# Optimization experiments

Hardware: AMD Instinct MI355X
Metric: run time of the kernel (lower is better)

Reference implementation:

```python
import jax, jax.numpy as jnp
import numpy as np
import math

B, S, D = 16, 2048, 64


def setup_inputs() -> dict:
    key = jax.random.key(0)
    k1, k2, k3 = jax.random.split(key, 3)
    Q = jax.random.normal(k1, (B, S, D), dtype=jnp.float32)
    K = jax.random.normal(k2, (B, S, D), dtype=jnp.float32)
    V = jax.random.normal(k3, (B, S, D), dtype=jnp.float32)
    # causal mask: True where attention is disallowed (strict upper triangle)
    mask = jnp.triu(jnp.ones((S, S), dtype=bool), k=1)
    mask = jnp.broadcast_to(mask, (B, S, S))
    return {"Q": Q, "K": K, "V": V, "mask": mask, "dk": 64}


def reference(Q, K, V, mask, dk):
    # w = Q K^T / sqrt(dk), masked fill with -1e8
    w = jnp.einsum("bqd,bkd->bqk", Q, K) / math.sqrt(dk)
    w = jnp.where(mask, jnp.float32(-1.0e8), w)
    # distance_func in the original returns 0 (constant, under no_grad),
    # so exp(-1e8 * 0) * w == w; output is softmax of masked scaled scores.
    distance_score = jnp.float32(0.0)
    s = jnp.exp(jnp.float32(-1.0e8) * distance_score) * w
    a = jax.nn.softmax(s, axis=-1)
    return a
```

## Files before the change

### kernel.cpp

```cpp
#include <hip/hip_runtime.h>

using bf16x8 = __attribute__((ext_vector_type(8))) short;
using u16x8  = __attribute__((ext_vector_type(8))) unsigned short;
using f32x4  = __attribute__((ext_vector_type(4))) float;

static constexpr int S  = 2048;
static constexpr int D  = 64;
static constexpr int TQ = 64;
static constexpr float QSCALE = 0.18033688f;

__device__ __forceinline__ unsigned short bf16_rne(float x) {
    unsigned u = __builtin_bit_cast(unsigned, x);
    u += 0x7FFFu + ((u >> 16) & 1u);
    return (unsigned short)(u >> 16);
}
__device__ __forceinline__ float bf16_f32(unsigned short h) {
    unsigned u = ((unsigned)h) << 16;
    return __builtin_bit_cast(float, u);
}
__device__ __forceinline__ f32x4 mfma16(bf16x8 a, bf16x8 b, f32x4 c) {
    return __builtin_amdgcn_mfma_f32_16x16x32_bf16(a, b, c, 0, 0, 0);
}
__device__ __forceinline__ void lbar() {
    asm volatile("s_waitcnt lgkmcnt(0)" ::: "memory");
    __builtin_amdgcn_s_barrier();
    asm volatile("" ::: "memory");
}

__global__ __launch_bounds__(512, 1)
void monotonic_attn(const float* __restrict__ Qg, const float* __restrict__ Kg,
                    float* __restrict__ out)
{
    __shared__ unsigned short qlds[8192];
    __shared__ unsigned short kls[8][2][1024];
    __shared__ float red[8][64];

    const int bid  = blockIdx.x;
    const int wid  = (bid & 7) * ((int)gridDim.x >> 3) + (bid >> 3);
    const int b    = wid >> 4;
    const int pair = wid & 15;

    const int tid = threadIdx.x, lane = tid & 63, wv = tid >> 6;
    const int l15 = lane & 15, g = lane >> 4;

    const float* __restrict__ Qb = Qg + (size_t)b * S * D;
    const float* __restrict__ Kb = Kg + (size_t)b * S * D;
    float* __restrict__ outb = out + (size_t)b * (size_t)S * S;

    const int srow  = lane >> 2;
    const int scp   = lane & 3;
    const int woff0 = srow * 64 + (((scp << 1)    ) ^ (srow & 7)) * 8;
    const int woff1 = srow * 64 + (((scp << 1) | 1) ^ (srow & 7)) * 8;
    const int roff0 = l15 * 64 + ((g    ) ^ (l15 & 7)) * 8;
    const int roff1 = l15 * 64 + ((4 | g) ^ (l15 & 7)) * 8;

    for (int half = 0; half < 2; ++half) {
        const int qt   = half ? pair : 31 - pair;
        const int q0   = qt * TQ;
        const int kend = q0 + TQ;
        const int nC   = kend >> 4;
        const int ni   = (nC - wv + 7) >> 3;

        lbar();
        {
            const int qrow = tid >> 3, qcp = tid & 7;
            const float4* src = reinterpret_cast<const float4*>(Qb + (size_t)(q0 + qrow) * D + qcp * 8);
            const float4 f0 = src[0], f1 = src[1];
            float v[8];
            *reinterpret_cast<float4*>(&v[0]) = f0;
            *reinterpret_cast<float4*>(&v[4]) = f1;
            u16x8 hv, lv;
            #pragma unroll
            for (int i = 0; i < 8; ++i) {
                const float s = v[i] * QSCALE;
                const unsigned short hb = bf16_rne(s);
                hv[i] = hb;
                lv[i] = bf16_rne(s - bf16_f32(hb));
            }
            const int off = qrow * 64 + (qcp ^ (qrow & 7)) * 8;
            *reinterpret_cast<u16x8*>(&qlds[off])        = hv;
            *reinterpret_cast<u16x8*>(&qlds[4096 + off]) = lv;
        }
        lbar();

        bf16x8 qhi[4][2], qlo[4][2];
        #pragma unroll
        for (int qs = 0; qs < 4; ++qs) {
            const int row = qs * 16 + l15;
            #pragma unroll
            for (int c = 0; c < 2; ++c) {
                const int off = row * 64 + ((((c << 2) | g)) ^ (row & 7)) * 8;
                qhi[qs][c] = *reinterpret_cast<const bf16x8*>(&qlds[off]);
                qlo[qs][c] = *reinterpret_cast<const bf16x8*>(&qlds[4096 + off]);
            }
        }

        float inv4[4];
        for (int pass = 0; pass < 2; ++pass) {
            float rsum[4] = {0.f, 0.f, 0.f, 0.f};

            float4 ra0, ra1, ra2, ra3, rb0, rb1, rb2, rb3;
            auto issueA = [&](int i) {
                const int c = wv + (i << 3);
                const float4* p4 = reinterpret_cast<const float4*>(Kb) + (c << 8) + (lane << 2);
                ra0 = p4[0]; ra1 = p4[1]; ra2 = p4[2]; ra3 = p4[3];
            };
            auto issueB = [&](int i) {
                const int c = wv + (i << 3);
                const float4* p4 = reinterpret_cast<const float4*>(Kb) + (c << 8) + (lane << 2);
                rb0 = p4[0]; rb1 = p4[1]; rb2 = p4[2]; rb3 = p4[3];
            };
            auto stage = [&](int i, const float4& x0, const float4& x1,
                             const float4& x2, const float4& x3) {
                float v[16];
                *reinterpret_cast<float4*>(&v[0])  = x0;
                *reinterpret_cast<float4*>(&v[4])  = x1;
                *reinterpret_cast<float4*>(&v[8])  = x2;
                *reinterpret_cast<float4*>(&v[12]) = x3;
                u16x8 h0, h1;
                #pragma unroll
                for (int j = 0; j < 8; ++j) {
                    h0[j] = bf16_rne(v[j]);
                    h1[j] = bf16_rne(v[8 + j]);
                }
                unsigned short* bp = &kls[wv][i & 1][0];
                *reinterpret_cast<u16x8*>(&bp[woff0]) = h0;
                *reinterpret_cast<u16x8*>(&bp[woff1]) = h1;
            };
            auto comp = [&](int i) {
                const unsigned short* bp = &kls[wv][i & 1][0];
                const bf16x8 kf0 = *reinterpret_cast<const bf16x8*>(&bp[roff0]);
                const bf16x8 kf1 = *reinterpret_cast<const bf16x8*>(&bp[roff1]);
                const int klo = (wv + (i << 3)) << 4;
                const int kb  = klo + g * 4;
                #pragma unroll
                for (int qs = 0; qs < 4; ++qs) {
                    const int qmin = q0 + qs * 16, qg = qmin + l15;
                    if (pass == 0) {
                        if (klo > qmin + 15) continue;
                        f32x4 acc = {0.f, 0.f, 0.f, 0.f};
                        acc = mfma16(kf0, qhi[qs][0], acc);
                        acc = mfma16(kf1, qhi[qs][1], acc);
                        acc = mfma16(kf0, qlo[qs][0], acc);
                        acc = mfma16(kf1, qlo[qs][1], acc);
                        if (klo + 15 <= qmin) {
                            rsum[qs] += exp2f(acc[0]) + exp2f(acc[1]) + exp2f(acc[2]) + exp2f(acc[3]);
                        } else {
                            #pragma unroll
                            for (int r = 0; r < 4; ++r)
                                rsum[qs] += (kb + r <= qg) ? exp2f(acc[r]) : 0.f;
                        }
                    } else {
                        f32x4 ov = {0.f, 0.f, 0.f, 0.f};
                        if (klo <= qmin + 15) {
                            f32x4 acc = {0.f, 0.f, 0.f, 0.f};
                            acc = mfma16(kf0, qhi[qs][0], acc);
                            acc = mfma16(kf1, qhi[qs][1], acc);
                            acc = mfma16(kf0, qlo[qs][0], acc);
                            acc = mfma16(kf1, qlo[qs][1], acc);
                            if (klo + 15 <= qmin) {
                                ov[0] = exp2f(acc[0]) * inv4[qs];
                                ov[1] = exp2f(acc[1]) * inv4[qs];
                                ov[2] = exp2f(acc[2]) * inv4[qs];
                                ov[3] = exp2f(acc[3]) * inv4[qs];
                            } else {
                                ov[0] = (kb + 0 <= qg) ? exp2f(acc[0]) * inv4[qs] : 0.f;
                                ov[1] = (kb + 1 <= qg) ? exp2f(acc[1]) * inv4[qs] : 0.f;
                                ov[2] = (kb + 2 <= qg) ? exp2f(acc[2]) * inv4[qs] : 0.f;
                                ov[3] = (kb + 3 <= qg) ? exp2f(acc[3]) * inv4[qs] : 0.f;
                            }
                        }
                        *reinterpret_cast<f32x4*>(outb + (size_t)qg * S + kb) = ov;
                    }
                }
            };

            if (ni > 0) issueA(0);
            if (ni > 1) issueB(1);
            int i = 0;
            for (; i + 2 <= ni; i += 2) {
                stage(i, ra0, ra1, ra2, ra3);
                if (i + 2 < ni) issueA(i + 2);
                comp(i);
                stage(i + 1, rb0, rb1, rb2, rb3);
                if (i + 3 < ni) issueB(i + 3);
                comp(i + 1);
            }
            if (i < ni) { stage(i, ra0, ra1, ra2, ra3); comp(i); }

            if (pass == 0) {
                #pragma unroll
                for (int qs = 0; qs < 4; ++qs) {
                    float v = rsum[qs];
                    v += __shfl_xor(v, 16);
                    v += __shfl_xor(v, 32);
                    if (g == 0) red[wv][qs * 16 + l15] = v;
                }
                lbar();
                #pragma unroll
                for (int qs = 0; qs < 4; ++qs) {
                    const int qi = qs * 16 + l15;
                    inv4[qs] = 1.f / (red[0][qi] + red[1][qi] + red[2][qi] + red[3][qi]
                                    + red[4][qi] + red[5][qi] + red[6][qi] + red[7][qi]);
                }
            }
        }

        {
            f32x4 z = {0.f, 0.f, 0.f, 0.f};
            const size_t rb = (size_t)(q0 + (tid >> 3)) * S;
            for (int cc = kend + (tid & 7) * 4; cc < S; cc += 32)
                *reinterpret_cast<f32x4*>(&outb[rb + cc]) = z;
        }
    }
}

extern "C" void kernel_launch(void* const* d_in, const int* in_sizes, int n_in,
                              void* d_out, int out_size, void* d_ws, size_t ws_size,
                              hipStream_t stream)
{
    const float* Q = (const float*)d_in[0];
    const float* K = (const float*)d_in[1];
    float* out     = (float*)d_out;
    const int nb   = in_sizes[0] / (S * D);

    monotonic_attn<<<dim3(nb * 16), dim3(512), 0, stream>>>(Q, K, out);
}
```

Baseline: 67.43 us.

## Process 32-key chunks per wave iteration and use nontemporal output stores

Each wave now stages and computes two 16-key subtiles (32 keys) per iteration instead of one. This doubles the K loads in flight and halves the loop and barrier overhead per key. The output stores, including the zero fill of the masked region, become nontemporal so the large streaming output does not pollute the caches. The cost is higher register and LDS use, plus coarser causal-boundary granularity that adds some wasted work on diagonal chunks.

```diff
diff --git a/kernel.cpp b/kernel.cpp
--- a/kernel.cpp
+++ b/kernel.cpp
@@ -32,7 +32,7 @@
                     float* __restrict__ out)
 {
     __shared__ unsigned short qlds[8192];
-    __shared__ unsigned short kls[8][2][1024];
+    __shared__ unsigned short kls[8][2][2048];
     __shared__ float red[8][64];
 
     const int bid  = blockIdx.x;
@@ -51,14 +51,20 @@
     const int scp   = lane & 3;
     const int woff0 = srow * 64 + (((scp << 1)    ) ^ (srow & 7)) * 8;
     const int woff1 = srow * 64 + (((scp << 1) | 1) ^ (srow & 7)) * 8;
-    const int roff0 = l15 * 64 + ((g    ) ^ (l15 & 7)) * 8;
-    const int roff1 = l15 * 64 + ((4 | g) ^ (l15 & 7)) * 8;
+    int koff[2][2];
+    #pragma unroll
+    for (int s2 = 0; s2 < 2; ++s2) {
+        const int row = s2 * 16 + l15;
+        koff[s2][0] = row * 64 + ((g    ) ^ (row & 7)) * 8;
+        koff[s2][1] = row * 64 + ((4 | g) ^ (row & 7)) * 8;
+    }
 
     for (int half = 0; half < 2; ++half) {
         const int qt   = half ? pair : 31 - pair;
         const int q0   = qt * TQ;
+        const int qmax = q0 + 63;
         const int kend = q0 + TQ;
-        const int nC   = kend >> 4;
+        const int nC   = kend >> 5;
         const int ni   = (nC - wv + 7) >> 3;
 
         lbar();
@@ -99,78 +105,118 @@
         for (int pass = 0; pass < 2; ++pass) {
             float rsum[4] = {0.f, 0.f, 0.f, 0.f};
 
-            float4 ra0, ra1, ra2, ra3, rb0, rb1, rb2, rb3;
+            float4 ra0, ra1, ra2, ra3, ra4, ra5, ra6, ra7;
+            float4 rb0, rb1, rb2, rb3, rb4, rb5, rb6, rb7;
             auto issueA = [&](int i) {
                 const int c = wv + (i << 3);
-                const float4* p4 = reinterpret_cast<const float4*>(Kb) + (c << 8) + (lane << 2);
-                ra0 = p4[0]; ra1 = p4[1]; ra2 = p4[2]; ra3 = p4[3];
+                const float4* p = reinterpret_cast<const float4*>(Kb) + ((size_t)c << 9) + (lane << 2);
+                ra0 = p[0]; ra1 = p[1]; ra2 = p[2]; ra3 = p[3];
+                ra4 = p[256]; ra5 = p[257]; ra6 = p[258]; ra7 = p[259];
             };
             auto issueB = [&](int i) {
                 const int c = wv + (i << 3);
-                const float4* p4 = reinterpret_cast<const float4*>(Kb) + (c << 8) + (lane << 2);
-                rb0 = p4[0]; rb1 = p4[1]; rb2 = p4[2]; rb3 = p4[3];
+                const float4* p = reinterpret_cast<const float4*>(Kb) + ((size_t)c << 9) + (lane << 2);
+                rb0 = p[0]; rb1 = p[1]; rb2 = p[2]; rb3 = p[3];
+                rb4 = p[256]; rb5 = p[257]; rb6 = p[258]; rb7 = p[259];
             };
             auto stage = [&](int i, const float4& x0, const float4& x1,
-                             const float4& x2, const float4& x3) {
+                             const float4& x2, const float4& x3,
+                             const float4& x4, const float4& x5,
+                             const float4& x6, const float4& x7) {
+                unsigned short* bp = &kls[wv][i & 1][0];
                 float v[16];
+                u16x8 h0, h1;
                 *reinterpret_cast<float4*>(&v[0])  = x0;
                 *reinterpret_cast<float4*>(&v[4])  = x1;
                 *reinterpret_cast<float4*>(&v[8])  = x2;
                 *reinterpret_cast<float4*>(&v[12]) = x3;
-                u16x8 h0, h1;
-                #pragma unroll
-                for (int j = 0; j < 8; ++j) {
-                    h0[j] = bf16_rne(v[j]);
-                    h1[j] = bf16_rne(v[8 + j]);
-                }
-                unsigned short* bp = &kls[wv][i & 1][0];
+                #pragma unroll
+                for (int j = 0; j < 8; ++j) { h0[j] = bf16_rne(v[j]); h1[j] = bf16_rne(v[8 + j]); }
                 *reinterpret_cast<u16x8*>(&bp[woff0]) = h0;
                 *reinterpret_cast<u16x8*>(&bp[woff1]) = h1;
+                *reinterpret_cast<float4*>(&v[0])  = x4;
+                *reinterpret_cast<float4*>(&v[4])  = x5;
+                *reinterpret_cast<float4*>(&v[8])  = x6;
+                *reinterpret_cast<float4*>(&v[12]) = x7;
+                #pragma unroll
+                for (int j = 0; j < 8; ++j) { h0[j] = bf16_rne(v[j]); h1[j] = bf16_rne(v[8 + j]); }
+                *reinterpret_cast<u16x8*>(&bp[woff0 + 1024]) = h0;
+                *reinterpret_cast<u16x8*>(&bp[woff1 + 1024]) = h1;
             };
             auto comp = [&](int i) {
                 const unsigned short* bp = &kls[wv][i & 1][0];
-                const bf16x8 kf0 = *reinterpret_cast<const bf16x8*>(&bp[roff0]);
-                const bf16x8 kf1 = *reinterpret_cast<const bf16x8*>(&bp[roff1]);
-                const int klo = (wv + (i << 3)) << 4;
-                const int kb  = klo + g * 4;
+                const bf16x8 k00 = *reinterpret_cast<const bf16x8*>(&bp[koff[0][0]]);
+                const bf16x8 k01 = *reinterpret_cast<const bf16x8*>(&bp[koff[0][1]]);
+                const bf16x8 k10 = *reinterpret_cast<const bf16x8*>(&bp[koff[1][0]]);
+                const bf16x8 k11 = *reinterpret_cast<const bf16x8*>(&bp[koff[1][1]]);
+                const int kbase = (wv + (i << 3)) << 5;
                 #pragma unroll
                 for (int qs = 0; qs < 4; ++qs) {
                     const int qmin = q0 + qs * 16, qg = qmin + l15;
                     if (pass == 0) {
-                        if (klo > qmin + 15) continue;
-                        f32x4 acc = {0.f, 0.f, 0.f, 0.f};
-                        acc = mfma16(kf0, qhi[qs][0], acc);
-                        acc = mfma16(kf1, qhi[qs][1], acc);
-                        acc = mfma16(kf0, qlo[qs][0], acc);
-                        acc = mfma16(kf1, qlo[qs][1], acc);
-                        if (klo + 15 <= qmin) {
-                            rsum[qs] += exp2f(acc[0]) + exp2f(acc[1]) + exp2f(acc[2]) + exp2f(acc[3]);
-                        } else {
-                            #pragma unroll
-                            for (int r = 0; r < 4; ++r)
-                                rsum[qs] += (kb + r <= qg) ? exp2f(acc[r]) : 0.f;
-                        }
-                    } else {
-                        f32x4 ov = {0.f, 0.f, 0.f, 0.f};
-                        if (klo <= qmin + 15) {
+                        #pragma unroll
+                        for (int s2 = 0; s2 < 2; ++s2) {
+                            const int klo = kbase + s2 * 16;
+                            if (klo > qmin + 15) continue;
+                            const bf16x8 kf0 = s2 ? k10 : k00;
+                            const bf16x8 kf1 = s2 ? k11 : k01;
                             f32x4 acc = {0.f, 0.f, 0.f, 0.f};
                             acc = mfma16(kf0, qhi[qs][0], acc);
                             acc = mfma16(kf1, qhi[qs][1], acc);
                             acc = mfma16(kf0, qlo[qs][0], acc);
                             acc = mfma16(kf1, qlo[qs][1], acc);
                             if (klo + 15 <= qmin) {
-                                ov[0] = exp2f(acc[0]) * inv4[qs];
-                                ov[1] = exp2f(acc[1]) * inv4[qs];
-                                ov[2] = exp2f(acc[2]) * inv4[qs];
-                                ov[3] = exp2f(acc[3]) * inv4[qs];
+                                rsum[qs] += exp2f(acc[0]) + exp2f(acc[1]) + exp2f(acc[2]) + exp2f(acc[3]);
                             } else {
-                                ov[0] = (kb + 0 <= qg) ? exp2f(acc[0]) * inv4[qs] : 0.f;
-                                ov[1] = (kb + 1 <= qg) ? exp2f(acc[1]) * inv4[qs] : 0.f;
-                                ov[2] = (kb + 2 <= qg) ? exp2f(acc[2]) * inv4[qs] : 0.f;
-                                ov[3] = (kb + 3 <= qg) ? exp2f(acc[3]) * inv4[qs] : 0.f;
+                                const int kb = klo + g * 4;
+                                #pragma unroll
+                                for (int r = 0; r < 4; ++r)
+                                    rsum[qs] += (kb + r <= qg) ? exp2f(acc[r]) : 0.f;
                             }
                         }
-                        *reinterpret_cast<f32x4*>(outb + (size_t)qg * S + kb) = ov;
+                    } else {
+                        f32x4 ov0 = {0.f, 0.f, 0.f, 0.f}, ov1 = {0.f, 0.f, 0.f, 0.f};
+                        if (kbase <= qmin + 15) {
+                            f32x4 acc = {0.f, 0.f, 0.f, 0.f};
+                            acc = mfma16(k00, qhi[qs][0], acc);
+                            acc = mfma16(k01, qhi[qs][1], acc);
+                            acc = mfma16(k00, qlo[qs][0], acc);
+                            acc = mfma16(k01, qlo[qs][1], acc);
+                            if (kbase + 15 <= qmin) {
+                                ov0[0] = exp2f(acc[0]) * inv4[qs];
+                                ov0[1] = exp2f(acc[1]) * inv4[qs];
+                                ov0[2] = exp2f(acc[2]) * inv4[qs];
+                                ov0[3] = exp2f(acc[3]) * inv4[qs];
+                            } else {
+                                const int kb = kbase + g * 4;
+                                ov0[0] = (kb + 0 <= qg) ? exp2f(acc[0]) * inv4[qs] : 0.f;
+                                ov0[1] = (kb + 1 <= qg) ? exp2f(acc[1]) * inv4[qs] : 0.f;
+                                ov0[2] = (kb + 2 <= qg) ? exp2f(acc[2]) * inv4[qs] : 0.f;
+                                ov0[3] = (kb + 3 <= qg) ? exp2f(acc[3]) * inv4[qs] : 0.f;
+                            }
+                        }
+                        if (kbase + 16 <= qmin + 15) {
+                            f32x4 acc = {0.f, 0.f, 0.f, 0.f};
+                            acc = mfma16(k10, qhi[qs][0], acc);
+                            acc = mfma16(k11, qhi[qs][1], acc);
+                            acc = mfma16(k10, qlo[qs][0], acc);
+                            acc = mfma16(k11, qlo[qs][1], acc);
+                            if (kbase + 31 <= qmin) {
+                                ov1[0] = exp2f(acc[0]) * inv4[qs];
+                                ov1[1] = exp2f(acc[1]) * inv4[qs];
+                                ov1[2] = exp2f(acc[2]) * inv4[qs];
+                                ov1[3] = exp2f(acc[3]) * inv4[qs];
+                            } else {
+                                const int kb = kbase + 16 + g * 4;
+                                ov1[0] = (kb + 0 <= qg) ? exp2f(acc[0]) * inv4[qs] : 0.f;
+                                ov1[1] = (kb + 1 <= qg) ? exp2f(acc[1]) * inv4[qs] : 0.f;
+                                ov1[2] = (kb + 2 <= qg) ? exp2f(acc[2]) * inv4[qs] : 0.f;
+                                ov1[3] = (kb + 3 <= qg) ? exp2f(acc[3]) * inv4[qs] : 0.f;
+                            }
+                        }
+                        float* rowp = outb + (size_t)qg * S + kbase + g * 4;
+                        __builtin_nontemporal_store(ov0, reinterpret_cast<f32x4*>(rowp));
+                        __builtin_nontemporal_store(ov1, reinterpret_cast<f32x4*>(rowp + 16));
                     }
                 }
             };
@@ -179,14 +225,14 @@
             if (ni > 1) issueB(1);
             int i = 0;
             for (; i + 2 <= ni; i += 2) {
-                stage(i, ra0, ra1, ra2, ra3);
+                stage(i, ra0, ra1, ra2, ra3, ra4, ra5, ra6, ra7);
                 if (i + 2 < ni) issueA(i + 2);
                 comp(i);
-                stage(i + 1, rb0, rb1, rb2, rb3);
+                stage(i + 1, rb0, rb1, rb2, rb3, rb4, rb5, rb6, rb7);
                 if (i + 3 < ni) issueB(i + 3);
                 comp(i + 1);
             }
-            if (i < ni) { stage(i, ra0, ra1, ra2, ra3); comp(i); }
+            if (i < ni) { stage(i, ra0, ra1, ra2, ra3, ra4, ra5, ra6, ra7); comp(i); }
 
             if (pass == 0) {
                 #pragma unroll
@@ -210,7 +256,7 @@
             f32x4 z = {0.f, 0.f, 0.f, 0.f};
             const size_t rb = (size_t)(q0 + (tid >> 3)) * S;
             for (int cc = kend + (tid & 7) * 4; cc < S; cc += 32)
-                *reinterpret_cast<f32x4*>(&outb[rb + cc]) = z;
+                __builtin_nontemporal_store(z, reinterpret_cast<f32x4*>(&outb[rb + cc]));
         }
     }
 }
```

Measured after the change: 98.02 us. +45.4%, slower.

## Drop split-bf16 Q correction and remap key chunks to adjacent pairs per wave

Applied to the files above, without the earlier changes.

Stores Q only as a single rounded bf16 value instead of a hi/lo split pair, which halves the MFMA count per score tile and the Q LDS footprint. Key chunks are now assigned to waves in adjacent pairs (2*wv, 2*wv+1, then a stride of 16) rather than a stride of 8, which changes the write locality of output rows and the load balance across waves. The change gives up the extra precision of the lo correction term, so scores are computed at plain bf16 accuracy. This risks larger softmax error.

```diff
diff --git a/kernel.cpp b/kernel.cpp
--- a/kernel.cpp
+++ b/kernel.cpp
@@ -14,10 +14,6 @@
     u += 0x7FFFu + ((u >> 16) & 1u);
     return (unsigned short)(u >> 16);
 }
-__device__ __forceinline__ float bf16_f32(unsigned short h) {
-    unsigned u = ((unsigned)h) << 16;
-    return __builtin_bit_cast(float, u);
-}
 __device__ __forceinline__ f32x4 mfma16(bf16x8 a, bf16x8 b, f32x4 c) {
     return __builtin_amdgcn_mfma_f32_16x16x32_bf16(a, b, c, 0, 0, 0);
 }
@@ -31,7 +27,7 @@
 void monotonic_attn(const float* __restrict__ Qg, const float* __restrict__ Kg,
                     float* __restrict__ out)
 {
-    __shared__ unsigned short qlds[8192];
+    __shared__ unsigned short qlds[4096];
     __shared__ unsigned short kls[8][2][1024];
     __shared__ float red[8][64];
 
@@ -54,12 +50,14 @@
     const int roff0 = l15 * 64 + ((g    ) ^ (l15 & 7)) * 8;
     const int roff1 = l15 * 64 + ((4 | g) ^ (l15 & 7)) * 8;
 
+    auto cidx = [&](int i) { return 2 * wv + ((i >> 1) << 4) + (i & 1); };
+
     for (int half = 0; half < 2; ++half) {
         const int qt   = half ? pair : 31 - pair;
         const int q0   = qt * TQ;
         const int kend = q0 + TQ;
         const int nC   = kend >> 4;
-        const int ni   = (nC - wv + 7) >> 3;
+        const int ni   = (nC > 2 * wv) ? (((nC - 2 * wv + 15) >> 4) << 1) : 0;
 
         lbar();
         {
@@ -69,29 +67,22 @@
             float v[8];
             *reinterpret_cast<float4*>(&v[0]) = f0;
             *reinterpret_cast<float4*>(&v[4]) = f1;
-            u16x8 hv, lv;
+            u16x8 hv;
             #pragma unroll
-            for (int i = 0; i < 8; ++i) {
-                const float s = v[i] * QSCALE;
-                const unsigned short hb = bf16_rne(s);
-                hv[i] = hb;
-                lv[i] = bf16_rne(s - bf16_f32(hb));
-            }
+            for (int i = 0; i < 8; ++i) hv[i] = bf16_rne(v[i] * QSCALE);
             const int off = qrow * 64 + (qcp ^ (qrow & 7)) * 8;
-            *reinterpret_cast<u16x8*>(&qlds[off])        = hv;
-            *reinterpret_cast<u16x8*>(&qlds[4096 + off]) = lv;
+            *reinterpret_cast<u16x8*>(&qlds[off]) = hv;
         }
         lbar();
 
-        bf16x8 qhi[4][2], qlo[4][2];
+        bf16x8 qf[4][2];
         #pragma unroll
         for (int qs = 0; qs < 4; ++qs) {
             const int row = qs * 16 + l15;
             #pragma unroll
             for (int c = 0; c < 2; ++c) {
                 const int off = row * 64 + ((((c << 2) | g)) ^ (row & 7)) * 8;
-                qhi[qs][c] = *reinterpret_cast<const bf16x8*>(&qlds[off]);
-                qlo[qs][c] = *reinterpret_cast<const bf16x8*>(&qlds[4096 + off]);
+                qf[qs][c] = *reinterpret_cast<const bf16x8*>(&qlds[off]);
             }
         }
 
@@ -101,13 +92,11 @@
 
             float4 ra0, ra1, ra2, ra3, rb0, rb1, rb2, rb3;
             auto issueA = [&](int i) {
-                const int c = wv + (i << 3);
-                const float4* p4 = reinterpret_cast<const float4*>(Kb) + (c << 8) + (lane << 2);
+                const float4* p4 = reinterpret_cast<const float4*>(Kb) + (cidx(i) << 8) + (lane << 2);
                 ra0 = p4[0]; ra1 = p4[1]; ra2 = p4[2]; ra3 = p4[3];
             };
             auto issueB = [&](int i) {
-                const int c = wv + (i << 3);
-                const float4* p4 = reinterpret_cast<const float4*>(Kb) + (c << 8) + (lane << 2);
+                const float4* p4 = reinterpret_cast<const float4*>(Kb) + (cidx(i) << 8) + (lane << 2);
                 rb0 = p4[0]; rb1 = p4[1]; rb2 = p4[2]; rb3 = p4[3];
             };
             auto stage = [&](int i, const float4& x0, const float4& x1,
@@ -131,7 +120,7 @@
                 const unsigned short* bp = &kls[wv][i & 1][0];
                 const bf16x8 kf0 = *reinterpret_cast<const bf16x8*>(&bp[roff0]);
                 const bf16x8 kf1 = *reinterpret_cast<const bf16x8*>(&bp[roff1]);
-                const int klo = (wv + (i << 3)) << 4;
+                const int klo = cidx(i) << 4;
                 const int kb  = klo + g * 4;
                 #pragma unroll
                 for (int qs = 0; qs < 4; ++qs) {
@@ -139,10 +128,8 @@
                     if (pass == 0) {
                         if (klo > qmin + 15) continue;
                         f32x4 acc = {0.f, 0.f, 0.f, 0.f};
-                        acc = mfma16(kf0, qhi[qs][0], acc);
-                        acc = mfma16(kf1, qhi[qs][1], acc);
-                        acc = mfma16(kf0, qlo[qs][0], acc);
-                        acc = mfma16(kf1, qlo[qs][1], acc);
+                        acc = mfma16(kf0, qf[qs][0], acc);
+                        acc = mfma16(kf1, qf[qs][1], acc);
                         if (klo + 15 <= qmin) {
                             rsum[qs] += exp2f(acc[0]) + exp2f(acc[1]) + exp2f(acc[2]) + exp2f(acc[3]);
                         } else {
@@ -154,10 +141,8 @@
                         f32x4 ov = {0.f, 0.f, 0.f, 0.f};
                         if (klo <= qmin + 15) {
                             f32x4 acc = {0.f, 0.f, 0.f, 0.f};
-                            acc = mfma16(kf0, qhi[qs][0], acc);
-                            acc = mfma16(kf1, qhi[qs][1], acc);
-                            acc = mfma16(kf0, qlo[qs][0], acc);
-                            acc = mfma16(kf1, qlo[qs][1], acc);
+                            acc = mfma16(kf0, qf[qs][0], acc);
+                            acc = mfma16(kf1, qf[qs][1], acc);
                             if (klo + 15 <= qmin) {
                                 ov[0] = exp2f(acc[0]) * inv4[qs];
                                 ov[1] = exp2f(acc[1]) * inv4[qs];
```

Result: slower. 72.34 us (+7.3%).
